# Kernel tuning notes

Measured on AMD Instinct MI355X. Metric: run time of the kernel, lower is better.

## Reference

```python
import jax, jax.numpy as jnp
import numpy as np
from jax import lax

S, T = 128, 32768            # seq_len (tokens), token_size (samples per token)
K, STRIDE = 1024, 512        # kernel/fourier size, stride
HE, HD, C = 1024, 1024, 1024 # enc_hidden, dec_hidden, output classes
NW = (T - K) // STRIDE + 1   # 63 windows per token

_WIN_IDX = np.arange(NW)[:, None] * STRIDE + np.arange(K)  # (NW, K)

def strided_fourier(x):
    # x: (..., T) -> real part of FFT over each strided window: (..., NW, K)
    w = x[..., _WIN_IDX]
    return jnp.fft.fft(w, axis=-1).real.astype(x.dtype)

def _lstm_cell(h, c, gates, H):
    # torch gate order: i, f, g, o
    i = jax.nn.sigmoid(gates[..., 0:H])
    f = jax.nn.sigmoid(gates[..., H:2 * H])
    g = jnp.tanh(gates[..., 2 * H:3 * H])
    o = jax.nn.sigmoid(gates[..., 3 * H:4 * H])
    c = f * c + i * g
    h = o * jnp.tanh(c)
    return h, c


def setup_inputs() -> dict:
    key = jax.random.key(0)
    ks = jax.random.split(key, 13)
    def n(k, shape, s=0.02):
        return (jax.random.normal(k, shape, jnp.float32) * s)
    return {
        "x": jax.random.normal(ks[0], (S, T), jnp.float32),
        "Wih_e": n(ks[1], (4 * HE, K)), "Whh_e": n(ks[2], (4 * HE, HE)), "b_e": n(ks[3], (4 * HE,)),
        "Wm1": n(ks[4], (HE, HE)), "bm1": n(ks[5], (HE,)),
        "Wm2": n(ks[6], (HD, HE)), "bm2": n(ks[7], (HD,)),
        "Wih_d": n(ks[8], (4 * HD, K)), "Whh_d": n(ks[9], (4 * HD, HD)), "b_d": n(ks[10], (4 * HD,)),
        "Wo": n(ks[11], (C, HD)), "bo": n(ks[12], (C,)),
    }


def reference(x, Wih_e, Whh_e, b_e, Wm1, bm1, Wm2, bm2, Wih_d, Whh_d, b_d, Wo, bo):
    # --- strided FFT features (dropout=0 -> identity) ---
    fouriers = strided_fourier(x)  # (S, NW, K)

    # --- encoder LSTM: batch=S, time=NW ---
    def enc_step(carry, xt):  # xt: (S, K)
        h, c = carry
        gates = xt @ Wih_e.T + h @ Whh_e.T + b_e
        return _lstm_cell(h, c, gates, HE), None
    z = jnp.zeros((S, HE), x.dtype)
    (h_enc, _), _ = lax.scan(enc_step, (z, z), jnp.swapaxes(fouriers, 0, 1))

    # --- mid linear on final hidden: Linear->ReLU->Linear->Tanh ---
    h_mid = jnp.tanh(jax.nn.relu(h_enc @ Wm1.T + bm1) @ Wm2.T + bm2)  # (S, HD)
    h0 = h_mid[0]  # (HD,); torch code uses h for both h and c init

    # --- decoder: sequential over tokens, hidden carried across steps ---
    def outer(carry, fw):  # fw: (NW, K)
        def inner(hc, xt):  # xt: (K,)
            h, c = hc
            gates = xt @ Wih_d.T + h @ Whh_d.T + b_d
            return _lstm_cell(h, c, gates, HD), None
        (h, c), _ = lax.scan(inner, carry, fw)
        # dec_output[-1] == final hidden h
        out = jax.nn.log_softmax(h @ Wo.T + bo, axis=0)  # (C,)
        return (h, c), out

    _, outputs = lax.scan(outer, (h0, h0), fouriers)
    return outputs  # (S, C)
```

## Files before the change

### kernel.cpp

```cpp
#include <hip/hip_runtime.h>

typedef unsigned short u16;
typedef unsigned u32;
typedef unsigned long long u64;
typedef __bf16 bf16x8 __attribute__((ext_vector_type(8)));
typedef _Float16 half8 __attribute__((ext_vector_type(8)));
typedef float f32x4 __attribute__((ext_vector_type(4)));

__device__ __forceinline__ u16 f2b(float f) {
  unsigned u = __builtin_bit_cast(unsigned, f);
  u = (u + 0x7FFFu + ((u >> 16) & 1u)) >> 16;
  return (u16)u;
}
__device__ __forceinline__ float b2f(u16 h) {
  return __builtin_bit_cast(float, ((unsigned)h) << 16);
}
__device__ __forceinline__ u16 f2h(float f) {
  _Float16 h = (_Float16)f;
  return __builtin_bit_cast(unsigned short, h);
}
__device__ __forceinline__ float sigmoidf_(float x) { return 1.0f / (1.0f + expf(-x)); }
__device__ __forceinline__ float fsig(float x) {
  x = fminf(fmaxf(x, -30.f), 30.f);
  return 1.0f / (1.0f + __expf(-x));
}
__device__ __forceinline__ float ftanh_(float x) {
  x = fminf(fmaxf(x, -15.f), 15.f);
  float e = __expf(2.0f * x);
  return (e - 1.0f) / (e + 1.0f);
}
__device__ __forceinline__ u64 aload(const u64* p) {
  return __hip_atomic_load(p, __ATOMIC_RELAXED, __HIP_MEMORY_SCOPE_AGENT);
}

template <int EPI, bool OUTBF, bool ACC, bool SLAB = false>
__global__ __launch_bounds__(256) void gemm_bt(
    const u16* __restrict__ A, int lda,
    const u16* __restrict__ B, int ldb,
    void* __restrict__ Cout, int ldc,
    const float* __restrict__ bias,
    int M, int N, int K) {
  __shared__ __align__(16) u16 As[64 * 40];
  __shared__ __align__(16) u16 Bs[64 * 40];
  const int t = threadIdx.x;
  const int n0 = blockIdx.x * 64, m0 = blockIdx.y * 64;
  const int wave = t >> 6, lane = t & 63;
  const int wm = (wave >> 1) * 32, wn = (wave & 1) * 32;
  const int quad = lane >> 4, r16 = lane & 15;
  const int srow = t >> 2, scol = (t & 3) * 8;
  f32x4 acc[2][2] = {};
  const u16* ap = A + (size_t)(m0 + srow) * lda + scol;
  const u16* bp = B + (size_t)(n0 + srow) * ldb + scol;
  for (int k0 = 0; k0 < K; k0 += 32) {
    uint4 av = *(const uint4*)(ap + k0);
    uint4 bv = *(const uint4*)(bp + k0);
    __syncthreads();
    *(uint4*)&As[srow * 40 + scol] = av;
    *(uint4*)&Bs[srow * 40 + scol] = bv;
    __syncthreads();
    bf16x8 a0 = *(const bf16x8*)&As[(wm + r16) * 40 + quad * 8];
    bf16x8 a1 = *(const bf16x8*)&As[(wm + 16 + r16) * 40 + quad * 8];
    bf16x8 b0 = *(const bf16x8*)&Bs[(wn + r16) * 40 + quad * 8];
    bf16x8 b1 = *(const bf16x8*)&Bs[(wn + 16 + r16) * 40 + quad * 8];
    acc[0][0] = __builtin_amdgcn_mfma_f32_16x16x32_bf16(a0, b0, acc[0][0], 0, 0, 0);
    acc[0][1] = __builtin_amdgcn_mfma_f32_16x16x32_bf16(a0, b1, acc[0][1], 0, 0, 0);
    acc[1][0] = __builtin_amdgcn_mfma_f32_16x16x32_bf16(a1, b0, acc[1][0], 0, 0, 0);
    acc[1][1] = __builtin_amdgcn_mfma_f32_16x16x32_bf16(a1, b1, acc[1][1], 0, 0, 0);
  }
  for (int mi = 0; mi < 2; mi++)
    for (int ni = 0; ni < 2; ni++)
      for (int r = 0; r < 4; r++) {
        int gm = m0 + wm + mi * 16 + quad * 4 + r;
        int gn = n0 + wn + ni * 16 + r16;
        float v = acc[mi][ni][r];
        size_t idx;
        if (SLAB) {
          int q = gn >> 10, bb = (gn >> 5) & 31, jj = gn & 31;
          idx = ((size_t)bb * 8064 + gm) * 128 + q * 32 + jj;
        } else {
          idx = (size_t)gm * ldc + gn;
        }
        if (ACC) v += ((float*)Cout)[idx];
        if (bias) v += bias[gn];
        if (EPI == 1) v = fmaxf(v, 0.0f);
        if (EPI == 2) v = tanhf(v);
        if (OUTBF) ((u16*)Cout)[idx] = f2b(v);
        else ((float*)Cout)[idx] = v;
      }
}

__global__ __launch_bounds__(256) void k_cos(u16* __restrict__ Chi, u16* __restrict__ Clo) {
  int gid = blockIdx.x * 256 + threadIdx.x;
  int k = gid >> 10, n = gid & 1023;
  int m = (k * n) & 1023;
  float c = cospif((float)m * (1.0f / 512.0f));
  u16 hi = f2b(c);
  Chi[gid] = hi;
  Clo[gid] = f2b(c - b2f(hi));
}

__global__ __launch_bounds__(256) void k_win(const float* __restrict__ x,
                                             u16* __restrict__ Whi, u16* __restrict__ Wlo) {
  int gid = blockIdx.x * 256 + threadIdx.x;
  int e = gid * 4;
  int r = e >> 10, n = e & 1023;
  int wI = r >> 7, s = r & 127;
  const float* src = x + (size_t)s * 32768 + wI * 512 + n;
  float4 v = *(const float4*)src;
  float vv[4] = {v.x, v.y, v.z, v.w};
#pragma unroll
  for (int i = 0; i < 4; i++) {
    u16 hi = f2b(vv[i]);
    Whi[e + i] = hi;
    Wlo[e + i] = f2b(vv[i] - b2f(hi));
  }
}

__global__ __launch_bounds__(256) void k_f2bk(const float* __restrict__ src, u16* __restrict__ dst) {
  int gid = blockIdx.x * 256 + threadIdx.x;
  int i = gid * 4;
  float4 v = *(const float4*)(src + i);
  dst[i] = f2b(v.x); dst[i + 1] = f2b(v.y); dst[i + 2] = f2b(v.z); dst[i + 3] = f2b(v.w);
}

__global__ __launch_bounds__(256) void k_perm(const u16* __restrict__ F1, u16* __restrict__ F2) {
  int gid = blockIdx.x * 256 + threadIdx.x;
  int ro = gid >> 7, n8 = (gid & 127) * 8;
  int s = ro / 63, wI = ro % 63;
  *(uint4*)&F2[(size_t)ro * 1024 + n8] = *(const uint4*)&F1[(size_t)(wI * 128 + s) * 1024 + n8];
}

__global__ __launch_bounds__(256) void k_cell_enc(const float* __restrict__ g,
                                                  const u16* __restrict__ gihe, int t0,
                                                  float* __restrict__ c_e,
                                                  u16* __restrict__ At) {
  int gid = blockIdx.x * 256 + threadIdx.x;
  int s = gid >> 10, j = gid & 1023;
  const float* gr = g + (size_t)s * 4096;
  const u16* er = gihe + (size_t)(t0 * 128 + s) * 4096;
  float iv = sigmoidf_(gr[j] + b2f(er[j]));
  float fv = sigmoidf_(gr[j + 1024] + b2f(er[j + 1024]));
  float gv = tanhf(gr[j + 2048] + b2f(er[j + 2048]));
  float ov = sigmoidf_(gr[j + 3072] + b2f(er[j + 3072]));
  float c = fv * c_e[gid] + iv * gv;
  c_e[gid] = c;
  At[(size_t)s * 1024 + j] = f2b(ov * tanhf(c));
}

__global__ void k_initdec(const float* __restrict__ hmid, u64* __restrict__ hb) {
  int gid = blockIdx.x * blockDim.x + threadIdx.x;
  if (gid < 512) {
    u32 lo = (u32)f2h(hmid[2 * gid]) | ((u32)f2h(hmid[2 * gid + 1]) << 16);
    hb[gid] = (u64)lo;
  } else if (gid < 1024) {
    hb[gid] = 0xFFFFFFFF00000000ull;
  }
}

__global__ __launch_bounds__(256, 1) void dec_persist(
    const float* __restrict__ Whh, const u16* __restrict__ GihS,
    const float* __restrict__ hmid,
    u64* __restrict__ hb, float* __restrict__ hfinal) {
  const int b = blockIdx.x, t = threadIdx.x;
  const int w = t >> 6, lane = t & 63;
  const int quad = lane >> 4, r16 = lane & 15;

  half8 afrag[8][8];
#pragma unroll
  for (int mt = 0; mt < 8; mt++) {
    int lr = mt * 16 + r16;
    int q = lr >> 5, jj = lr & 31;
    const float* Wr = Whh + (size_t)(q * 1024 + b * 32 + jj) * 1024 + 256 * w + quad * 8;
#pragma unroll
    for (int ks = 0; ks < 8; ks++) {
      half8 v;
#pragma unroll
      for (int j = 0; j < 8; j++) v[j] = (_Float16)Wr[ks * 32 + j];
      afrag[mt][ks] = v;
    }
  }

  __shared__ __align__(16) u32 hsu[512];
  __shared__ float gpart[2][4][128];
  __shared__ __align__(16) u16 uslab[2][2048];

  {
    uint4 g0 = *(const uint4*)(GihS + (size_t)b * 8064 * 128 + t * 8);
    *(uint4*)&uslab[0][t * 8] = g0;
  }
  float cst = (t < 32) ? hmid[b * 32 + t] : 0.0f;

  int n = 0;
  for (int s = 0; s < 128; s++) {
    for (int wI = 0; wI < 63; wI++, n++) {
      const u32 tn = (u32)n;
      const u64* p = hb + (size_t)(n & 1) * 512 + 2 * t;
      u64 v0, v1;
      for (;;) {
        v0 = aload(p);
        v1 = aload(p + 1);
        if (((u32)(v0 >> 32) == tn) & ((u32)(v1 >> 32) == tn)) break;
      }
      ((u64*)hsu)[t] = (v0 & 0xFFFFFFFFull) | (v1 << 32);

      const bool slabload = (n & 15) == 0;
      uint4 gsv;
      if (slabload) {
        int nn = (n + 16 <= 8048) ? n + 16 : 8048;
        gsv = *(const uint4*)(GihS + ((size_t)b * 8064 + nn) * 128 + t * 8);
      }

      f32x4 acc[8];
#pragma unroll
      for (int mt = 0; mt < 8; mt++) acc[mt] = (f32x4){0.f, 0.f, 0.f, 0.f};
      const int kb = 128 * w;
#pragma unroll
      for (int ks = 0; ks < 8; ks++) {
        half8 bfrag = *(const half8*)&hsu[kb + 16 * ks + 4 * quad];
#pragma unroll
        for (int mt = 0; mt < 8; mt++)
          acc[mt] = __builtin_amdgcn_mfma_f32_16x16x32_f16(afrag[mt][ks], bfrag, acc[mt], 0, 0, 0);
      }
      if (r16 == 0) {
#pragma unroll
        for (int mt = 0; mt < 8; mt++)
          *(f32x4*)&gpart[n & 1][w][mt * 16 + 4 * quad] = acc[mt];
      }
      __syncthreads();
      if (slabload) *(uint4*)&uslab[((n >> 4) + 1) & 1][t * 8] = gsv;
      if (t < 32) {
        const int pb = n & 1, sb = (n >> 4) & 1, so = (n & 15) * 128;
        float gi = gpart[pb][0][t] + gpart[pb][1][t] + gpart[pb][2][t] + gpart[pb][3][t];
        float gf = gpart[pb][0][32 + t] + gpart[pb][1][32 + t] + gpart[pb][2][32 + t] + gpart[pb][3][32 + t];
        float gg = gpart[pb][0][64 + t] + gpart[pb][1][64 + t] + gpart[pb][2][64 + t] + gpart[pb][3][64 + t];
        float go = gpart[pb][0][96 + t] + gpart[pb][1][96 + t] + gpart[pb][2][96 + t] + gpart[pb][3][96 + t];
        gi += b2f(uslab[sb][so + t]);
        gf += b2f(uslab[sb][so + 32 + t]);
        gg += b2f(uslab[sb][so + 64 + t]);
        go += b2f(uslab[sb][so + 96 + t]);
        float iv = fsig(gi), fv = fsig(gf), gv = ftanh_(gg), ov = fsig(go);
        cst = fv * cst + iv * gv;
        float h = ov * ftanh_(cst);
        u32 h16 = (u32)f2h(h);
        u32 oth = (u32)__shfl_down((int)h16, 1);
        if ((t & 1) == 0) {
          u64 word = ((u64)(u32)(n + 1) << 32) | (h16 | (oth << 16));
          __hip_atomic_store(&hb[(size_t)((n + 1) & 1) * 512 + b * 16 + (t >> 1)], word,
                             __ATOMIC_RELAXED, __HIP_MEMORY_SCOPE_AGENT);
        }
        if (wI == 62) hfinal[(size_t)s * 1024 + b * 32 + t] = h;
      }
    }
  }
}

__global__ __launch_bounds__(256) void k_lsm(const float* __restrict__ logits, float* __restrict__ out) {
  int s = blockIdx.x, t = threadIdx.x;
  const float* L = logits + (size_t)s * 1024;
  __shared__ float red[4], red2[4];
  float m = -1e30f;
  for (int i = t; i < 1024; i += 256) m = fmaxf(m, L[i]);
  for (int o = 1; o < 64; o <<= 1) m = fmaxf(m, __shfl_xor(m, o));
  if ((t & 63) == 0) red[t >> 6] = m;
  __syncthreads();
  m = fmaxf(fmaxf(red[0], red[1]), fmaxf(red[2], red[3]));
  float sum = 0.f;
  for (int i = t; i < 1024; i += 256) sum += expf(L[i] - m);
  for (int o = 1; o < 64; o <<= 1) sum += __shfl_xor(sum, o);
  if ((t & 63) == 0) red2[t >> 6] = sum;
  __syncthreads();
  sum = red2[0] + red2[1] + red2[2] + red2[3];
  float lse = m + logf(sum);
  for (int i = t; i < 1024; i += 256) out[(size_t)s * 1024 + i] = L[i] - lse;
}

extern "C" void kernel_launch(void* const* d_in, const int* in_sizes, int n_in,
                              void* d_out, int out_size, void* d_ws, size_t ws_size,
                              hipStream_t stream) {
  const float* x     = (const float*)d_in[0];
  const float* Wih_e = (const float*)d_in[1];
  const float* Whh_e = (const float*)d_in[2];
  const float* b_e   = (const float*)d_in[3];
  const float* Wm1   = (const float*)d_in[4];
  const float* bm1   = (const float*)d_in[5];
  const float* Wm2   = (const float*)d_in[6];
  const float* bm2   = (const float*)d_in[7];
  const float* Wih_d = (const float*)d_in[8];
  const float* Whh_d = (const float*)d_in[9];
  const float* b_d   = (const float*)d_in[10];
  const float* Wo    = (const float*)d_in[11];
  const float* bo    = (const float*)d_in[12];
  float* out = (float*)d_out;

  char* w = (char*)d_ws;
  size_t off = 0;
  auto alloc = [&](size_t bytes) { size_t r = off; off += (bytes + 255) & ~(size_t)255; return r; };
  u16* Chi = (u16*)(w + alloc((size_t)1024 * 1024 * 2));
  u16* Clo = (u16*)(w + alloc((size_t)1024 * 1024 * 2));
  u16* F1  = (u16*)(w + alloc((size_t)8064 * 1024 * 2));
  char* f2slot = w + alloc((size_t)8064 * 1024 * 2);
  u16* WinHi = (u16*)f2slot;
  u16* F2    = (u16*)f2slot;
  u16* WinLo = (u16*)(w + alloc((size_t)8064 * 1024 * 2));
  char* gislot = w + alloc((size_t)8064 * 4096 * 2);
  float* Fgem = (float*)gislot;
  u16* GihS   = (u16*)gislot;
  u16* Gihe = (u16*)(w + alloc((size_t)8064 * 4096 * 2));
  u16* Wihd  = (u16*)(w + alloc((size_t)4096 * 1024 * 2));
  u16* Wihe  = (u16*)(w + alloc((size_t)4096 * 1024 * 2));
  u16* Whhe  = (u16*)(w + alloc((size_t)4096 * 1024 * 2));
  u16* Wm1b = (u16*)(w + alloc((size_t)1024 * 1024 * 2));
  u16* Wm2b = (u16*)(w + alloc((size_t)1024 * 1024 * 2));
  u16* Wob  = (u16*)(w + alloc((size_t)1024 * 1024 * 2));
  u16* At   = (u16*)(w + alloc((size_t)128 * 1024 * 2));
  float* Ge = (float*)(w + alloc((size_t)128 * 4096 * 4));
  float* Ce = (float*)(w + alloc((size_t)128 * 1024 * 4));
  u16* Mid1 = (u16*)(w + alloc((size_t)128 * 1024 * 2));
  float* Hmid = (float*)(w + alloc((size_t)128 * 1024 * 4));
  u64* Hb = (u64*)(w + alloc((size_t)1024 * 8));
  float* Hfin = (float*)(w + alloc((size_t)128 * 1024 * 4));
  u16* Hfinb  = (u16*)(w + alloc((size_t)128 * 1024 * 2));
  float* Logit = (float*)(w + alloc((size_t)128 * 1024 * 4));
  (void)ws_size; (void)in_sizes; (void)n_in; (void)out_size;

  hipMemsetAsync(At, 0, (size_t)128 * 1024 * 2, stream);
  hipMemsetAsync(Ce, 0, (size_t)128 * 1024 * 4, stream);

  k_cos<<<4096, 256, 0, stream>>>(Chi, Clo);
  k_win<<<8064, 256, 0, stream>>>(x, WinHi, WinLo);
  gemm_bt<0, false, false><<<dim3(16, 126), 256, 0, stream>>>(WinHi, 1024, Chi, 1024, Fgem, 1024, nullptr, 8064, 1024, 1024);
  gemm_bt<0, false, true><<<dim3(16, 126), 256, 0, stream>>>(WinHi, 1024, Clo, 1024, Fgem, 1024, nullptr, 8064, 1024, 1024);
  gemm_bt<0, false, true><<<dim3(16, 126), 256, 0, stream>>>(WinLo, 1024, Chi, 1024, Fgem, 1024, nullptr, 8064, 1024, 1024);
  k_f2bk<<<8064, 256, 0, stream>>>(Fgem, F1);
  k_perm<<<4032, 256, 0, stream>>>(F1, F2);

  k_f2bk<<<4096, 256, 0, stream>>>(Wih_d, Wihd);
  k_f2bk<<<4096, 256, 0, stream>>>(Wih_e, Wihe);
  k_f2bk<<<4096, 256, 0, stream>>>(Whh_e, Whhe);
  k_f2bk<<<1024, 256, 0, stream>>>(Wm1, Wm1b);
  k_f2bk<<<1024, 256, 0, stream>>>(Wm2, Wm2b);
  k_f2bk<<<1024, 256, 0, stream>>>(Wo, Wob);

  gemm_bt<0, true, false, true><<<dim3(64, 126), 256, 0, stream>>>(F2, 1024, Wihd, 1024, GihS, 128, b_d, 8064, 4096, 1024);
  gemm_bt<0, true, false><<<dim3(64, 126), 256, 0, stream>>>(F1, 1024, Wihe, 1024, Gihe, 4096, b_e, 8064, 4096, 1024);

  for (int t = 0; t < 63; t++) {
    gemm_bt<0, false, false><<<dim3(64, 2), 256, 0, stream>>>(At, 1024, Whhe, 1024, Ge, 4096, nullptr, 128, 4096, 1024);
    k_cell_enc<<<512, 256, 0, stream>>>(Ge, Gihe, t, Ce, At);
  }

  gemm_bt<1, true, false><<<dim3(16, 2), 256, 0, stream>>>(At, 1024, Wm1b, 1024, Mid1, 1024, bm1, 128, 1024, 1024);
  gemm_bt<2, false, false><<<dim3(16, 2), 256, 0, stream>>>(Mid1, 1024, Wm2b, 1024, Hmid, 1024, bm2, 128, 1024, 1024);

  k_initdec<<<4, 256, 0, stream>>>(Hmid, Hb);
  dec_persist<<<32, 256, 0, stream>>>(Whh_d, GihS, Hmid, Hb, Hfin);

  k_f2bk<<<128, 256, 0, stream>>>(Hfin, Hfinb);
  gemm_bt<0, false, false><<<dim3(16, 2), 256, 0, stream>>>(Hfinb, 1024, Wob, 1024, Logit, 1024, bo, 128, 1024, 1024);
  k_lsm<<<128, 256, 0, stream>>>(Logit, out);
}
```

Baseline: 18.17 ms.

## Pin decoder blocks to one XCD and poll hidden state via L2

The persistent decoder now launches 256 blocks. Each reads its XCD id from a hardware register, and the first 32 blocks that land on one XCD are kept while the rest exit. A runtime probe checks that non-coherent sc0 loads and stores still see each other's writes through that XCD's shared L2. If the probe passes, the per-step hidden-state exchange uses plain sc0 global loads and stores instead of device-scope atomics, aiming to cut cross-block synchronisation latency on the 8064-step sequential chain. This adds a startup election and probe phase and relies on undocumented hardware-register and cache behaviour, with a fallback to the atomic path.

```diff
diff --git a/kernel.cpp b/kernel.cpp
--- a/kernel.cpp
+++ b/kernel.cpp
@@ -6,6 +6,8 @@
 typedef __bf16 bf16x8 __attribute__((ext_vector_type(8)));
 typedef _Float16 half8 __attribute__((ext_vector_type(8)));
 typedef float f32x4 __attribute__((ext_vector_type(4)));
+typedef unsigned uint4v __attribute__((ext_vector_type(4)));
+typedef unsigned uint2v __attribute__((ext_vector_type(2)));
 
 __device__ __forceinline__ u16 f2b(float f) {
   unsigned u = __builtin_bit_cast(unsigned, f);
@@ -31,6 +33,23 @@
 }
 __device__ __forceinline__ u64 aload(const u64* p) {
   return __hip_atomic_load(p, __ATOMIC_RELAXED, __HIP_MEMORY_SCOPE_AGENT);
+}
+
+__device__ __forceinline__ void l2_poll2(const u64* p, u64& a, u64& b) {
+  uint4v r;
+  asm volatile("global_load_dwordx4 %0, %1, off sc0\n\ts_waitcnt vmcnt(0)"
+               : "=&v"(r) : "v"(p) : "memory");
+  a = ((u64)r.y << 32) | (u64)r.x;
+  b = ((u64)r.w << 32) | (u64)r.z;
+}
+__device__ __forceinline__ u64 l2_load1(const u64* p) {
+  uint2v r;
+  asm volatile("global_load_dwordx2 %0, %1, off sc0\n\ts_waitcnt vmcnt(0)"
+               : "=&v"(r) : "v"(p) : "memory");
+  return ((u64)r.y << 32) | (u64)r.x;
+}
+__device__ __forceinline__ void l2_store(u64* p, u64 v) {
+  asm volatile("global_store_dwordx2 %0, %1, off sc0" :: "v"(p), "v"(v) : "memory");
 }
 
 template <int EPI, bool OUTBF, bool ACC, bool SLAB = false>
@@ -147,7 +166,9 @@
   At[(size_t)s * 1024 + j] = f2b(ov * tanhf(c));
 }
 
-__global__ void k_initdec(const float* __restrict__ hmid, u64* __restrict__ hb) {
+__global__ void k_initdec(const float* __restrict__ hmid, u64* __restrict__ hb,
+                          int* __restrict__ ctrl, u64* __restrict__ probe,
+                          u32* __restrict__ verdict) {
   int gid = blockIdx.x * blockDim.x + threadIdx.x;
   if (gid < 512) {
     u32 lo = (u32)f2h(hmid[2 * gid]) | ((u32)f2h(hmid[2 * gid + 1]) << 16);
@@ -155,13 +176,65 @@
   } else if (gid < 1024) {
     hb[gid] = 0xFFFFFFFF00000000ull;
   }
+  if (gid < 9) ctrl[gid] = (gid == 8) ? -1 : 0;
+  if (gid >= 16 && gid < 48) probe[gid - 16] = 0ull;
+  if (gid >= 48 && gid < 80) verdict[gid - 48] = 0u;
 }
 
 __global__ __launch_bounds__(256, 1) void dec_persist(
     const float* __restrict__ Whh, const u16* __restrict__ GihS,
     const float* __restrict__ hmid,
-    u64* __restrict__ hb, float* __restrict__ hfinal) {
-  const int b = blockIdx.x, t = threadIdx.x;
+    u64* __restrict__ hb, float* __restrict__ hfinal,
+    int* __restrict__ ctrl, u64* __restrict__ probe, u32* __restrict__ verdict) {
+  const int t = threadIdx.x;
+  u32 xcd = __builtin_amdgcn_s_getreg(63508) & 7u;
+  __shared__ int sslot;
+  if (t == 0) {
+    int tk = atomicAdd(&ctrl[xcd], 1);
+    if (tk == 31) atomicCAS(&ctrl[8], -1, (int)xcd);
+    int ch;
+    do {
+      ch = __hip_atomic_load(&ctrl[8], __ATOMIC_RELAXED, __HIP_MEMORY_SCOPE_AGENT);
+    } while (ch < 0);
+    sslot = (xcd == (u32)ch && tk < 32) ? tk : -1;
+  }
+  __syncthreads();
+  const int b = sslot;
+  if (b < 0) return;
+
+  __shared__ int sok;
+  if (t == 0) sok = 1;
+  __syncthreads();
+  for (int r = 0; r < 8; r++) {
+    if (sok) {
+      if (t == 0) l2_store(&probe[b], (u64)(0xC0DE0000u + (u32)r));
+      if (t < 32) {
+        const u64 want = (u64)(0xC0DE0000u + (u32)r);
+        bool got = false;
+        int lim = (r == 0) ? 30000 : 4000;
+        for (int it = 0; it < lim; it++) {
+          if (l2_load1(&probe[t]) >= want) { got = true; break; }
+        }
+        if (!got) sok = 0;
+      }
+    }
+    __syncthreads();
+  }
+  if (t == 0)
+    __hip_atomic_store(&verdict[b], sok ? 2u : 1u, __ATOMIC_RELAXED, __HIP_MEMORY_SCOPE_AGENT);
+  __shared__ int modef;
+  if (t == 0) modef = 2;
+  __syncthreads();
+  if (t < 32) {
+    u32 v;
+    do {
+      v = __hip_atomic_load(&verdict[t], __ATOMIC_RELAXED, __HIP_MEMORY_SCOPE_AGENT);
+    } while (v == 0);
+    if (v != 2) atomicMin(&modef, 1);
+  }
+  __syncthreads();
+  const bool fast = (modef == 2);
+
   const int w = t >> 6, lane = t & 63;
   const int quad = lane >> 4, r16 = lane & 15;
 
@@ -196,10 +269,17 @@
       const u32 tn = (u32)n;
       const u64* p = hb + (size_t)(n & 1) * 512 + 2 * t;
       u64 v0, v1;
-      for (;;) {
-        v0 = aload(p);
-        v1 = aload(p + 1);
-        if (((u32)(v0 >> 32) == tn) & ((u32)(v1 >> 32) == tn)) break;
+      if (fast) {
+        for (;;) {
+          l2_poll2(p, v0, v1);
+          if (((u32)(v0 >> 32) == tn) & ((u32)(v1 >> 32) == tn)) break;
+        }
+      } else {
+        for (;;) {
+          v0 = aload(p);
+          v1 = aload(p + 1);
+          if (((u32)(v0 >> 32) == tn) & ((u32)(v1 >> 32) == tn)) break;
+        }
       }
       ((u64*)hsu)[t] = (v0 & 0xFFFFFFFFull) | (v1 << 32);
 
@@ -245,8 +325,9 @@
         u32 oth = (u32)__shfl_down((int)h16, 1);
         if ((t & 1) == 0) {
           u64 word = ((u64)(u32)(n + 1) << 32) | (h16 | (oth << 16));
-          __hip_atomic_store(&hb[(size_t)((n + 1) & 1) * 512 + b * 16 + (t >> 1)], word,
-                             __ATOMIC_RELAXED, __HIP_MEMORY_SCOPE_AGENT);
+          u64* dst = &hb[(size_t)((n + 1) & 1) * 512 + b * 16 + (t >> 1)];
+          if (fast) l2_store(dst, word);
+          else __hip_atomic_store(dst, word, __ATOMIC_RELAXED, __HIP_MEMORY_SCOPE_AGENT);
         }
         if (wI == 62) hfinal[(size_t)s * 1024 + b * 32 + t] = h;
       }
@@ -318,6 +399,9 @@
   u16* Mid1 = (u16*)(w + alloc((size_t)128 * 1024 * 2));
   float* Hmid = (float*)(w + alloc((size_t)128 * 1024 * 4));
   u64* Hb = (u64*)(w + alloc((size_t)1024 * 8));
+  int* Ctrl = (int*)(w + alloc(256));
+  u64* Probe = (u64*)(w + alloc(256));
+  u32* Verdict = (u32*)(w + alloc(256));
   float* Hfin = (float*)(w + alloc((size_t)128 * 1024 * 4));
   u16* Hfinb  = (u16*)(w + alloc((size_t)128 * 1024 * 2));
   float* Logit = (float*)(w + alloc((size_t)128 * 1024 * 4));
@@ -352,8 +436,8 @@
   gemm_bt<1, true, false><<<dim3(16, 2), 256, 0, stream>>>(At, 1024, Wm1b, 1024, Mid1, 1024, bm1, 128, 1024, 1024);
   gemm_bt<2, false, false><<<dim3(16, 2), 256, 0, stream>>>(Mid1, 1024, Wm2b, 1024, Hmid, 1024, bm2, 128, 1024, 1024);
 
-  k_initdec<<<4, 256, 0, stream>>>(Hmid, Hb);
-  dec_persist<<<32, 256, 0, stream>>>(Whh_d, GihS, Hmid, Hb, Hfin);
+  k_initdec<<<4, 256, 0, stream>>>(Hmid, Hb, Ctrl, Probe, Verdict);
+  dec_persist<<<256, 256, 0, stream>>>(Whh_d, GihS, Hmid, Hb, Hfin, Ctrl, Probe, Verdict);
 
   k_f2bk<<<128, 256, 0, stream>>>(Hfin, Hfinb);
   gemm_bt<0, false, false><<<dim3(16, 2), 256, 0, stream>>>(Hfinb, 1024, Wob, 1024, Logit, 1024, bo, 128, 1024, 1024);
```

After: 17.41 ms. 4.1% less time.
